# Kernel tuning notes

Measured on AMD Instinct MI355X. Metric: run time of the kernel, lower is better.

Reference implementation:

```python
import jax, jax.numpy as jnp
import numpy as np

N_NODES = 8192
N_EDGES = 65536


def _segment_softmax(scores, seg_ids, num_segments):
    # scores: [E, 1], seg_ids: [E] -> softmax over edges sharing the same dst
    m = jax.ops.segment_max(scores, seg_ids, num_segments=num_segments)  # [N,1]
    e = jnp.exp(scores - m[seg_ids])
    denom = jax.ops.segment_sum(e, seg_ids, num_segments=num_segments)   # [N,1]
    return e / denom[seg_ids]


def setup_inputs() -> dict:
    key = jax.random.key(0)
    ks = jax.random.split(key, 12)
    s = lambda fin: 1.0 / np.sqrt(fin)
    inp = {
        'n_f': jax.random.normal(ks[0], (N_NODES, 1024), jnp.float32),
        'word2vec': jax.random.normal(ks[1], (N_NODES, 300), jnp.float32),
        's_f': jax.random.normal(ks[2], (N_EDGES, 16), jnp.float32),
        'src': jax.random.randint(ks[3], (N_EDGES,), 0, N_NODES),
        'dst': jax.random.randint(ks[4], (N_EDGES,), 0, N_NODES),
        'We': jax.random.normal(ks[5], (2064, 1024), jnp.float32) * s(2064),
        'be': jnp.zeros((1024,), jnp.float32),
        'Wel': jax.random.normal(ks[6], (600, 600), jnp.float32) * s(600),
        'bel': jnp.zeros((600,), jnp.float32),
        'Wa': jax.random.normal(ks[7], (1024, 1), jnp.float32) * s(1024),
        'ba': jnp.zeros((1,), jnp.float32),
        'Wal': jax.random.normal(ks[8], (600, 1), jnp.float32) * s(600),
        'bal': jnp.zeros((1,), jnp.float32),
        'Wn': jax.random.normal(ks[9], (2048, 1024), jnp.float32) * s(2048),
        'bn': jnp.zeros((1024,), jnp.float32),
        'Wnl': jax.random.normal(ks[10], (600, 300), jnp.float32) * s(600),
        'bnl': jnp.zeros((300,), jnp.float32),
    }
    return inp


def reference(n_f, word2vec, s_f, src, dst,
              We, be, Wel, bel, Wa, ba, Wal, bal, Wn, bn, Wnl, bnl):
    # ---- edge apply (H_H_EdgeApplyModule) ----
    src_nf = n_f[src]                                    # [E,1024] gather
    feat = jnp.concatenate([src_nf, s_f, n_f[dst]], axis=1)  # [E,2064]
    e_f = jax.nn.relu(feat @ We + be)                    # [E,1024]
    feat_lang = jnp.concatenate([word2vec[src], word2vec[dst]], axis=1)  # [E,600]
    e_f_lang = jax.nn.relu(feat_lang @ Wel + bel)        # [E,600]

    # ---- edge attention (E_AttentionModule1): scalar score per edge ----
    a_feat = e_f @ Wa + ba                               # [E,1]
    a_feat_lang = e_f_lang @ Wal + bal                   # [E,1]

    # ---- reduce: mailbox softmax over incoming edges per dst node ----
    alpha = _segment_softmax(a_feat, dst, N_NODES)       # [E,1]
    alpha_lang = _segment_softmax(a_feat_lang, dst, N_NODES)
    z_f = jax.ops.segment_sum(alpha * (src_nf + e_f), dst, num_segments=N_NODES)      # [N,1024]
    z_f_lang = jax.ops.segment_sum(alpha_lang * word2vec[src], dst, num_segments=N_NODES)  # [N,300]

    # ---- node apply (H_NodeApplyModule) ----
    new_n_f = jax.nn.relu(jnp.concatenate([n_f, z_f], axis=1) @ Wn + bn)              # [N,1024]
    new_n_f_lang = jax.nn.relu(jnp.concatenate([word2vec, z_f_lang], axis=1) @ Wnl + bnl)  # [N,300]
    return new_n_f, new_n_f_lang
```

## Files before the change

kernel.cpp:

```cpp
#include <hip/hip_runtime.h>
#include <hip/hip_bf16.h>

#define N_NODES 8192
#define N_EDGES 65536
#define OUT0_ELEMS ((size_t)N_NODES * 1024)

using bf16 = __hip_bfloat16;
typedef __attribute__((ext_vector_type(8))) short short8;
typedef __attribute__((ext_vector_type(4))) float f32x4;

__device__ __forceinline__ float b2f(bf16 x) { return __bfloat162float(x); }
__device__ __forceinline__ bf16 f2b(float x) { return __float2bfloat16(x); }
__device__ __forceinline__ unsigned short bbits(float x)
{
  union { bf16 h; unsigned short u; } v; v.h = f2b(x); return v.u;
}
__device__ __forceinline__ unsigned pack2(float a, float b)
{
  return (unsigned)bbits(a) | ((unsigned)bbits(b) << 16);
}
__device__ __forceinline__ float4 ld4b(const bf16* p)
{
  uint2 u = *(const uint2*)p;
  float4 r;
  r.x = __uint_as_float(u.x << 16);
  r.y = __uint_as_float(u.x & 0xffff0000u);
  r.z = __uint_as_float(u.y << 16);
  r.w = __uint_as_float(u.y & 0xffff0000u);
  return r;
}
__device__ __forceinline__ void st4b(bf16* p, float a, float b, float c, float d)
{
  uint2 v; v.x = pack2(a, b); v.y = pack2(c, d);
  *(uint2*)p = v;
}

__global__ void GNN_27650999451833_kernel() {}

__global__ void gnn6_zero(int* __restrict__ p, int n)
{
  int i = blockIdx.x * blockDim.x + threadIdx.x;
  if (i < n) p[i] = 0;
}

__global__ __launch_bounds__(256)
void gnn7_cvt(const float* __restrict__ src, bf16* __restrict__ dst, int n8)
{
  int i = blockIdx.x * blockDim.x + threadIdx.x;
  if (i < n8) {
    float4 a = ((const float4*)src)[2 * i];
    float4 b = ((const float4*)src)[2 * i + 1];
    uint4 p;
    p.x = pack2(a.x, a.y); p.y = pack2(a.z, a.w);
    p.z = pack2(b.x, b.y); p.w = pack2(b.z, b.w);
    ((uint4*)dst)[i] = p;
  }
}

__global__ __launch_bounds__(256)
void gnn8_pad_w2v(const float* __restrict__ src, bf16* __restrict__ dst)
{
  int idx = blockIdx.x * blockDim.x + threadIdx.x;
  if (idx >= N_NODES * 80) return;
  int r = idx / 80, c0 = (idx % 80) * 4;
  float v[4];
#pragma unroll
  for (int j = 0; j < 4; ++j) {
    int c = c0 + j;
    v[j] = (c < 300) ? src[(size_t)r * 300 + c] : 0.f;
  }
  uint2 p; p.x = pack2(v[0], v[1]); p.y = pack2(v[2], v[3]);
  *(uint2*)(dst + (size_t)r * 320 + c0) = p;
}

__global__ __launch_bounds__(256)
void gnn10_t_We(const float* __restrict__ src, bf16* __restrict__ dst)
{
  __shared__ float tile[32][33];
  const int kb = blockIdx.x * 32, nb = blockIdx.y * 32;
  const int tx = threadIdx.x & 31, ty = threadIdx.x >> 5;
  const int n = nb + tx;
#pragma unroll
  for (int i = ty; i < 32; i += 8)
    tile[i][tx] = (n < 1024)
        ? src[(size_t)(kb + i) * 1024 + n]
        : src[(size_t)(1040 + kb + i) * 1024 + (n - 1024)];
  __syncthreads();
#pragma unroll
  for (int i = ty; i < 32; i += 8)
    dst[(size_t)(nb + i) * 1024 + kb + tx] = f2b(tile[tx][i]);
}

__global__ __launch_bounds__(256)
void gnn10_t_Wn(const float* __restrict__ src, bf16* __restrict__ dst)
{
  __shared__ float tile[32][33];
  const int kb = blockIdx.x * 32, nb = blockIdx.y * 32;
  const int tx = threadIdx.x & 31, ty = threadIdx.x >> 5;
#pragma unroll
  for (int i = ty; i < 32; i += 8)
    tile[i][tx] = src[(size_t)(kb + i) * 1024 + nb + tx];
  __syncthreads();
#pragma unroll
  for (int i = ty; i < 32; i += 8)
    dst[(size_t)(nb + i) * 2048 + kb + tx] = f2b(tile[tx][i]);
}

__global__ __launch_bounds__(256)
void gnn10_t_Wel(const float* __restrict__ src, bf16* __restrict__ dst)
{
  __shared__ float tile[32][33];
  const int kb = blockIdx.x * 32, nb = blockIdx.y * 32;
  const int tx = threadIdx.x & 31, ty = threadIdx.x >> 5;
  const int n = nb + tx;
#pragma unroll
  for (int i = ty; i < 32; i += 8) {
    int k = kb + i;
    float v = 0.f;
    if (k < 300) {
      if (n < 600)       v = src[(size_t)k * 600 + n];
      else if (n < 1200) v = src[(size_t)(300 + k) * 600 + (n - 600)];
    }
    tile[i][tx] = v;
  }
  __syncthreads();
#pragma unroll
  for (int i = ty; i < 32; i += 8)
    dst[(size_t)(nb + i) * 320 + kb + tx] = f2b(tile[tx][i]);
}

__global__ __launch_bounds__(256)
void gnn10_t_Wnl(const float* __restrict__ src, bf16* __restrict__ dst)
{
  __shared__ float tile[32][33];
  const int kb = blockIdx.x * 32, nb = blockIdx.y * 32;
  const int tx = threadIdx.x & 31, ty = threadIdx.x >> 5;
  const int n = nb + tx;
#pragma unroll
  for (int i = ty; i < 32; i += 8) {
    int k = kb + i;
    int kr = (k < 300) ? k : ((k >= 320 && k < 620) ? (k - 20) : -1);
    tile[i][tx] = (kr >= 0 && n < 300) ? src[(size_t)kr * 300 + n] : 0.f;
  }
  __syncthreads();
#pragma unroll
  for (int i = ty; i < 32; i += 8)
    dst[(size_t)(nb + i) * 640 + kb + tx] = f2b(tile[tx][i]);
}

__global__ __launch_bounds__(256)
void gnn10_mm_P(const bf16* __restrict__ A, const bf16* __restrict__ BT,
                bf16* __restrict__ P)
{
  __shared__ short As[128 * 40];
  __shared__ short Bs[128 * 40];
  const int t = threadIdx.x;
  const int col0 = blockIdx.x * 128, row0 = blockIdx.y * 128;
  const int lane = t & 63, w = t >> 6, m16 = lane & 15, q = lane >> 4;
  const int wr = w >> 1, wc = w & 1;

  f32x4 acc[4][4];
#pragma unroll
  for (int mi = 0; mi < 4; ++mi)
#pragma unroll
    for (int ni = 0; ni < 4; ++ni) acc[mi][ni] = (f32x4){0.f, 0.f, 0.f, 0.f};

  const int ar = t >> 1, ah = (t & 1) * 16;
  const bf16* aptr = A + (size_t)(row0 + ar) * 1024 + ah;
  const bf16* bptr = BT + (size_t)(col0 + ar) * 1024 + ah;

  uint4 a0 = *(const uint4*)(aptr);
  uint4 a1 = *(const uint4*)(aptr + 8);
  uint4 b0 = *(const uint4*)(bptr);
  uint4 b1 = *(const uint4*)(bptr + 8);

  for (int k0 = 0; k0 < 1024; k0 += 32) {
    if (k0) __syncthreads();
    *(uint4*)&As[ar * 40 + ah] = a0;
    *(uint4*)&As[ar * 40 + ah + 8] = a1;
    *(uint4*)&Bs[ar * 40 + ah] = b0;
    *(uint4*)&Bs[ar * 40 + ah + 8] = b1;
    __syncthreads();
    if (k0 + 32 < 1024) {
      a0 = *(const uint4*)(aptr + k0 + 32);
      a1 = *(const uint4*)(aptr + k0 + 40);
      b0 = *(const uint4*)(bptr + k0 + 32);
      b1 = *(const uint4*)(bptr + k0 + 40);
    }
    short8 af[4];
#pragma unroll
    for (int mi = 0; mi < 4; ++mi)
      af[mi] = *(const short8*)&As[(wr * 64 + mi * 16 + m16) * 40 + 8 * q];
#pragma unroll
    for (int ni = 0; ni < 4; ++ni) {
      short8 bfv = *(const short8*)&Bs[(wc * 64 + ni * 16 + m16) * 40 + 8 * q];
#pragma unroll
      for (int mi = 0; mi < 4; ++mi)
        acc[mi][ni] =
            __builtin_amdgcn_mfma_f32_16x16x32_bf16(af[mi], bfv, acc[mi][ni], 0, 0, 0);
    }
  }
#pragma unroll
  for (int mi = 0; mi < 4; ++mi)
#pragma unroll
    for (int ni = 0; ni < 4; ++ni) {
      int c = col0 + wc * 64 + ni * 16 + m16;
#pragma unroll
      for (int r = 0; r < 4; ++r)
        P[(size_t)(row0 + wr * 64 + mi * 16 + 4 * q + r) * 2048 + c] =
            f2b(acc[mi][ni][r]);
    }
}

__global__ __launch_bounds__(256)
void gnn10_mm_out_n(const bf16* __restrict__ A0, const bf16* __restrict__ A1,
                    const bf16* __restrict__ BT, const float* __restrict__ bn,
                    float* __restrict__ out)
{
  __shared__ short As[128 * 40];
  __shared__ short Bs[128 * 40];
  const int t = threadIdx.x;
  const int col0 = blockIdx.x * 128, row0 = blockIdx.y * 128;
  const int lane = t & 63, w = t >> 6, m16 = lane & 15, q = lane >> 4;
  const int wr = w >> 1, wc = w & 1;

  f32x4 acc[4][4];
#pragma unroll
  for (int mi = 0; mi < 4; ++mi)
#pragma unroll
    for (int ni = 0; ni < 4; ++ni) acc[mi][ni] = (f32x4){0.f, 0.f, 0.f, 0.f};

  const int ar = t >> 1, ah = (t & 1) * 16;
  const bf16* ap0 = A0 + (size_t)(row0 + ar) * 1024 + ah;
  const bf16* ap1 = A1 + (size_t)(row0 + ar) * 1024 + ah;
  const bf16* bptr = BT + (size_t)(col0 + ar) * 2048 + ah;

  uint4 a0 = *(const uint4*)(ap0);
  uint4 a1 = *(const uint4*)(ap0 + 8);
  uint4 b0 = *(const uint4*)(bptr);
  uint4 b1 = *(const uint4*)(bptr + 8);

  for (int k0 = 0; k0 < 2048; k0 += 32) {
    if (k0) __syncthreads();
    *(uint4*)&As[ar * 40 + ah] = a0;
    *(uint4*)&As[ar * 40 + ah + 8] = a1;
    *(uint4*)&Bs[ar * 40 + ah] = b0;
    *(uint4*)&Bs[ar * 40 + ah + 8] = b1;
    __syncthreads();
    if (k0 + 32 < 2048) {
      int kn = k0 + 32;
      const bf16* ap = (kn < 1024) ? (ap0 + kn) : (ap1 + (kn - 1024));
      a0 = *(const uint4*)(ap);
      a1 = *(const uint4*)(ap + 8);
      b0 = *(const uint4*)(bptr + kn);
      b1 = *(const uint4*)(bptr + kn + 8);
    }
    short8 af[4];
#pragma unroll
    for (int mi = 0; mi < 4; ++mi)
      af[mi] = *(const short8*)&As[(wr * 64 + mi * 16 + m16) * 40 + 8 * q];
#pragma unroll
    for (int ni = 0; ni < 4; ++ni) {
      short8 bfv = *(const short8*)&Bs[(wc * 64 + ni * 16 + m16) * 40 + 8 * q];
#pragma unroll
      for (int mi = 0; mi < 4; ++mi)
        acc[mi][ni] =
            __builtin_amdgcn_mfma_f32_16x16x32_bf16(af[mi], bfv, acc[mi][ni], 0, 0, 0);
    }
  }
#pragma unroll
  for (int mi = 0; mi < 4; ++mi)
#pragma unroll
    for (int ni = 0; ni < 4; ++ni) {
      int c = col0 + wc * 64 + ni * 16 + m16;
      float bias = bn[c];
#pragma unroll
      for (int r = 0; r < 4; ++r) {
        float v = acc[mi][ni][r] + bias;
        out[(size_t)(row0 + wr * 64 + mi * 16 + 4 * q + r) * 1024 + c] =
            fmaxf(v, 0.f);
      }
    }
}

__global__ __launch_bounds__(256)
void gnn10_mm_Q(const bf16* __restrict__ A, const bf16* __restrict__ BT,
                bf16* __restrict__ Q)
{
  __shared__ short As[128 * 40];
  __shared__ short Bs[128 * 40];
  const int t = threadIdx.x;
  const int col0 = blockIdx.x * 128, row0 = blockIdx.y * 128;
  const int lane = t & 63, w = t >> 6, m16 = lane & 15, q = lane >> 4;
  const int wr = w >> 1, wc = w & 1;

  f32x4 acc[4][4];
#pragma unroll
  for (int mi = 0; mi < 4; ++mi)
#pragma unroll
    for (int ni = 0; ni < 4; ++ni) acc[mi][ni] = (f32x4){0.f, 0.f, 0.f, 0.f};

  const int ar = t >> 1, ah = (t & 1) * 16;
  const bf16* aptr = A + (size_t)(row0 + ar) * 320 + ah;
  const bf16* bptr = BT + (size_t)(col0 + ar) * 320 + ah;

  uint4 a0 = *(const uint4*)(aptr);
  uint4 a1 = *(const uint4*)(aptr + 8);
  uint4 b0 = *(const uint4*)(bptr);
  uint4 b1 = *(const uint4*)(bptr + 8);

  for (int k0 = 0; k0 < 320; k0 += 32) {
    if (k0) __syncthreads();
    *(uint4*)&As[ar * 40 + ah] = a0;
    *(uint4*)&As[ar * 40 + ah + 8] = a1;
    *(uint4*)&Bs[ar * 40 + ah] = b0;
    *(uint4*)&Bs[ar * 40 + ah + 8] = b1;
    __syncthreads();
    if (k0 + 32 < 320) {
      a0 = *(const uint4*)(aptr + k0 + 32);
      a1 = *(const uint4*)(aptr + k0 + 40);
      b0 = *(const uint4*)(bptr + k0 + 32);
      b1 = *(const uint4*)(bptr + k0 + 40);
    }
    short8 af[4];
#pragma unroll
    for (int mi = 0; mi < 4; ++mi)
      af[mi] = *(const short8*)&As[(wr * 64 + mi * 16 + m16) * 40 + 8 * q];
#pragma unroll
    for (int ni = 0; ni < 4; ++ni) {
      short8 bfv = *(const short8*)&Bs[(wc * 64 + ni * 16 + m16) * 40 + 8 * q];
#pragma unroll
      for (int mi = 0; mi < 4; ++mi)
        acc[mi][ni] =
            __builtin_amdgcn_mfma_f32_16x16x32_bf16(af[mi], bfv, acc[mi][ni], 0, 0, 0);
    }
  }
#pragma unroll
  for (int mi = 0; mi < 4; ++mi)
#pragma unroll
    for (int ni = 0; ni < 4; ++ni) {
      int c = col0 + wc * 64 + ni * 16 + m16;
#pragma unroll
      for (int r = 0; r < 4; ++r)
        Q[(size_t)(row0 + wr * 64 + mi * 16 + 4 * q + r) * 1280 + c] =
            f2b(acc[mi][ni][r]);
    }
}

__global__ __launch_bounds__(256)
void gnn10_mm_out_l(const bf16* __restrict__ A0, const bf16* __restrict__ A1,
                    const bf16* __restrict__ BT, const float* __restrict__ bnl,
                    float* __restrict__ out2)
{
  __shared__ short As[128 * 40];
  __shared__ short Bs[128 * 40];
  const int t = threadIdx.x;
  const int col0 = blockIdx.x * 128, row0 = blockIdx.y * 128;
  const int lane = t & 63, w = t >> 6, m16 = lane & 15, q = lane >> 4;
  const int wr = w >> 1, wc = w & 1;

  f32x4 acc[4][4];
#pragma unroll
  for (int mi = 0; mi < 4; ++mi)
#pragma unroll
    for (int ni = 0; ni < 4; ++ni) acc[mi][ni] = (f32x4){0.f, 0.f, 0.f, 0.f};

  const int ar = t >> 1, ah = (t & 1) * 16;
  const bf16* ap0 = A0 + (size_t)(row0 + ar) * 320 + ah;
  const bf16* ap1 = A1 + (size_t)(row0 + ar) * 320 + ah;
  const bf16* bptr = BT + (size_t)(col0 + ar) * 640 + ah;

  uint4 a0 = *(const uint4*)(ap0);
  uint4 a1 = *(const uint4*)(ap0 + 8);
  uint4 b0 = *(const uint4*)(bptr);
  uint4 b1 = *(const uint4*)(bptr + 8);

  for (int k0 = 0; k0 < 640; k0 += 32) {
    if (k0) __syncthreads();
    *(uint4*)&As[ar * 40 + ah] = a0;
    *(uint4*)&As[ar * 40 + ah + 8] = a1;
    *(uint4*)&Bs[ar * 40 + ah] = b0;
    *(uint4*)&Bs[ar * 40 + ah + 8] = b1;
    __syncthreads();
    if (k0 + 32 < 640) {
      int kn = k0 + 32;
      const bf16* ap = (kn < 320) ? (ap0 + kn) : (ap1 + (kn - 320));
      a0 = *(const uint4*)(ap);
      a1 = *(const uint4*)(ap + 8);
      b0 = *(const uint4*)(bptr + kn);
      b1 = *(const uint4*)(bptr + kn + 8);
    }
    short8 af[4];
#pragma unroll
    for (int mi = 0; mi < 4; ++mi)
      af[mi] = *(const short8*)&As[(wr * 64 + mi * 16 + m16) * 40 + 8 * q];
#pragma unroll
    for (int ni = 0; ni < 4; ++ni) {
      short8 bfv = *(const short8*)&Bs[(wc * 64 + ni * 16 + m16) * 40 + 8 * q];
#pragma unroll
      for (int mi = 0; mi < 4; ++mi)
        acc[mi][ni] =
            __builtin_amdgcn_mfma_f32_16x16x32_bf16(af[mi], bfv, acc[mi][ni], 0, 0, 0);
    }
  }
#pragma unroll
  for (int mi = 0; mi < 4; ++mi)
#pragma unroll
    for (int ni = 0; ni < 4; ++ni) {
      int c = col0 + wc * 64 + ni * 16 + m16;
      if (c < 300) {
        float bias = bnl[c];
#pragma unroll
        for (int r = 0; r < 4; ++r) {
          float v = acc[mi][ni][r] + bias;
          out2[(size_t)(row0 + wr * 64 + mi * 16 + 4 * q + r) * 300 + c] =
              fmaxf(v, 0.f);
        }
      }
    }
}

__global__ __launch_bounds__(256)
void gnn11_edge_score(const int* __restrict__ src, const int* __restrict__ dst,
                      const float* __restrict__ s_f, const float* __restrict__ We,
                      const float* __restrict__ be, const float* __restrict__ Wa,
                      const float* __restrict__ ba, const float* __restrict__ bel,
                      const float* __restrict__ Wal, const float* __restrict__ bal,
                      const bf16* __restrict__ P, const bf16* __restrict__ Q,
                      float* __restrict__ af, float* __restrict__ afl)
{
  const int t = threadIdx.x;
  const int lane = t & 63, w = t >> 6;
  const int c0 = 4 * t;
  const int e0 = blockIdx.x * 8;

  float wef[16][4];
#pragma unroll
  for (int k = 0; k < 16; ++k) {
    float4 v = *(const float4*)(We + (size_t)(1024 + k) * 1024 + c0);
    wef[k][0] = v.x; wef[k][1] = v.y; wef[k][2] = v.z; wef[k][3] = v.w;
  }
  float4 bev = *(const float4*)(be + c0);
  float4 wav = *(const float4*)(Wa + c0);
  const bool lact = (t < 150);
  float4 belv = {0, 0, 0, 0}, walv = {0, 0, 0, 0};
  if (lact) { belv = *(const float4*)(bel + c0); walv = *(const float4*)(Wal + c0); }

  int ss[8], dd[8];
  {
    int4 a = *(const int4*)(src + e0);
    int4 b = *(const int4*)(src + e0 + 4);
    ss[0] = a.x; ss[1] = a.y; ss[2] = a.z; ss[3] = a.w;
    ss[4] = b.x; ss[5] = b.y; ss[6] = b.z; ss[7] = b.w;
    int4 c = *(const int4*)(dst + e0);
    int4 d = *(const int4*)(dst + e0 + 4);
    dd[0] = c.x; dd[1] = c.y; dd[2] = c.z; dd[3] = c.w;
    dd[4] = d.x; dd[5] = d.y; dd[6] = d.z; dd[7] = d.w;
  }

  float pf[8], pl[8];

#pragma unroll
  for (int i = 0; i < 8; ++i) {
    const int e = e0 + i;

    float sfv[16];
    {
      const float4* sp = (const float4*)(s_f + (size_t)e * 16);
      float4 s0 = sp[0], s1 = sp[1], s2 = sp[2], s3 = sp[3];
      sfv[0] = s0.x; sfv[1] = s0.y; sfv[2] = s0.z; sfv[3] = s0.w;
      sfv[4] = s1.x; sfv[5] = s1.y; sfv[6] = s1.z; sfv[7] = s1.w;
      sfv[8] = s2.x; sfv[9] = s2.y; sfv[10] = s2.z; sfv[11] = s2.w;
      sfv[12] = s3.x; sfv[13] = s3.y; sfv[14] = s3.z; sfv[15] = s3.w;
    }

    float4 p1 = ld4b(P + (size_t)ss[i] * 2048 + c0);
    float4 p2 = ld4b(P + (size_t)dd[i] * 2048 + 1024 + c0);
    float pv[4] = {p1.x + p2.x + bev.x, p1.y + p2.y + bev.y,
                   p1.z + p2.z + bev.z, p1.w + p2.w + bev.w};
    float acc = 0.f;
#pragma unroll
    for (int j = 0; j < 4; ++j) {
      float v = pv[j];
#pragma unroll
      for (int k = 0; k < 16; ++k) v = fmaf(sfv[k], wef[k][j], v);
      acc = fmaf(fmaxf(v, 0.f), (&wav.x)[j], acc);
    }
    pf[i] = acc;
  }

#pragma unroll
  for (int i = 0; i < 8; ++i) {
    float acc = 0.f;
    if (lact) {
      float4 q1 = ld4b(Q + (size_t)ss[i] * 1280 + c0);
      float4 q2 = ld4b(Q + (size_t)dd[i] * 1280 + 600 + c0);
      float qv[4] = {q1.x + q2.x + belv.x, q1.y + q2.y + belv.y,
                     q1.z + q2.z + belv.z, q1.w + q2.w + belv.w};
#pragma unroll
      for (int j = 0; j < 4; ++j)
        acc = fmaf(fmaxf(qv[j], 0.f), (&walv.x)[j], acc);
    }
    pl[i] = acc;
  }

  __shared__ float shf[8][4], shl[8][4];
#pragma unroll
  for (int i = 0; i < 8; ++i) {
#pragma unroll
    for (int o = 32; o > 0; o >>= 1) {
      pf[i] += __shfl_down(pf[i], o, 64);
      pl[i] += __shfl_down(pl[i], o, 64);
    }
  }
  if (lane == 0) {
#pragma unroll
    for (int i = 0; i < 8; ++i) { shf[i][w] = pf[i]; shl[i][w] = pl[i]; }
  }
  __syncthreads();
  if (t < 8)
    af[e0 + t] = shf[t][0] + shf[t][1] + shf[t][2] + shf[t][3] + ba[0];
  if (t >= 64 && t < 72) {
    const int i = t & 7;
    afl[e0 + i] = shl[i][0] + shl[i][1] + shl[i][2] + shl[i][3] + bal[0];
  }
}

__global__ void gnn6_count(const int* __restrict__ dst, int* __restrict__ cnt)
{
  int e = blockIdx.x * blockDim.x + threadIdx.x;
  if (e < N_EDGES) atomicAdd(&cnt[dst[e]], 1);
}

__global__ __launch_bounds__(1024)
void gnn6_scan(const int* __restrict__ cnt, int* __restrict__ off, int* __restrict__ cur)
{
  __shared__ int sh[1024];
  const int t = threadIdx.x;
  int local[8]; int sum = 0;
#pragma unroll
  for (int i = 0; i < 8; ++i) { int v = cnt[t * 8 + i]; local[i] = sum; sum += v; }
  sh[t] = sum;
  __syncthreads();
  for (int d = 1; d < 1024; d <<= 1) {
    int v = (t >= d) ? sh[t - d] : 0;
    __syncthreads();
    sh[t] += v;
    __syncthreads();
  }
  int basev = (t > 0) ? sh[t - 1] : 0;
#pragma unroll
  for (int i = 0; i < 8; ++i) { int o = basev + local[i]; off[t * 8 + i] = o; cur[t * 8 + i] = o; }
  if (t == 1023) off[8192] = sh[1023];
}

__global__ void gnn6_fill(const int* __restrict__ dst, int* __restrict__ cur,
                          int* __restrict__ elist)
{
  int e = blockIdx.x * blockDim.x + threadIdx.x;
  if (e < N_EDGES) { int p = atomicAdd(&cur[dst[e]], 1); elist[p] = e; }
}

__global__ __launch_bounds__(256)
void gnn6_alpha(const int* __restrict__ off, const int* __restrict__ elist,
                float* __restrict__ af, float* __restrict__ afl)
{
  const int n = blockIdx.x * 256 + threadIdx.x;
  if (n >= N_NODES) return;
  const int base = off[n];
  const int deg = off[n + 1] - base;
  float m = -1e30f, ml = -1e30f;
  for (int i = 0; i < deg; ++i) {
    int e = elist[base + i];
    m = fmaxf(m, af[e]);
    ml = fmaxf(ml, afl[e]);
  }
  float den = 0.f, denl = 0.f;
  for (int i = 0; i < deg; ++i) {
    int e = elist[base + i];
    den += expf(af[e] - m);
    denl += expf(afl[e] - ml);
  }
  float inv = (den > 0.f) ? 1.f / den : 0.f;
  float invl = (denl > 0.f) ? 1.f / denl : 0.f;
  for (int i = 0; i < deg; ++i) {
    int e = elist[base + i];
    af[e] = expf(af[e] - m) * inv;
    afl[e] = expf(afl[e] - ml) * invl;
  }
}

__global__ __launch_bounds__(256)
void gnn9_node_z(const int* __restrict__ off, const int* __restrict__ elist,
                 const int* __restrict__ src, const float* __restrict__ af,
                 const float* __restrict__ afl, const bf16* __restrict__ nf_bf,
                 const bf16* __restrict__ w2v_pad, const float* __restrict__ s_f,
                 const float* __restrict__ We, const float* __restrict__ be,
                 const bf16* __restrict__ P, bf16* __restrict__ zf,
                 bf16* __restrict__ zfl_pad)
{
  const int node = blockIdx.x;
  const int t = threadIdx.x;
  const int c0 = 4 * t;
  const int base = off[node];
  const int deg = off[node + 1] - base;

  float wef[16][4];
#pragma unroll
  for (int k = 0; k < 16; ++k) {
    float4 v = *(const float4*)(We + (size_t)(1024 + k) * 1024 + c0);
    wef[k][0] = v.x; wef[k][1] = v.y; wef[k][2] = v.z; wef[k][3] = v.w;
  }
  float4 p2v = ld4b(P + (size_t)node * 2048 + 1024 + c0);
  float4 bev = *(const float4*)(be + c0);
  const float p2[4] = {p2v.x + bev.x, p2v.y + bev.y, p2v.z + bev.z, p2v.w + bev.w};

  float acc[4] = {0.f, 0.f, 0.f, 0.f};
  float accl[4] = {0.f, 0.f, 0.f, 0.f};
  const bool lact = (t < 75);

  for (int i = 0; i < deg; ++i) {
    const int e = elist[base + i];
    const int s = src[e];
    const float wgt = af[e];
    const float wl = afl[e];

    float sfv[16];
    {
      const float4* sp = (const float4*)(s_f + (size_t)e * 16);
      float4 s0 = sp[0], s1 = sp[1], s2 = sp[2], s3 = sp[3];
      sfv[0] = s0.x; sfv[1] = s0.y; sfv[2] = s0.z; sfv[3] = s0.w;
      sfv[4] = s1.x; sfv[5] = s1.y; sfv[6] = s1.z; sfv[7] = s1.w;
      sfv[8] = s2.x; sfv[9] = s2.y; sfv[10] = s2.z; sfv[11] = s2.w;
      sfv[12] = s3.x; sfv[13] = s3.y; sfv[14] = s3.z; sfv[15] = s3.w;
    }

    float4 p1 = ld4b(P + (size_t)s * 2048 + c0);
    float4 nf4 = ld4b(nf_bf + (size_t)s * 1024 + c0);
    const float p1a[4] = {p1.x, p1.y, p1.z, p1.w};
    const float nfa[4] = {nf4.x, nf4.y, nf4.z, nf4.w};
#pragma unroll
    for (int j = 0; j < 4; ++j) {
      float ef = p1a[j] + p2[j];
#pragma unroll
      for (int k = 0; k < 16; ++k) ef = fmaf(sfv[k], wef[k][j], ef);
      ef = fmaxf(ef, 0.f);
      acc[j] = fmaf(wgt, nfa[j] + ef, acc[j]);
    }
    if (lact) {
      float4 wv = ld4b(w2v_pad + (size_t)s * 320 + c0);
      accl[0] = fmaf(wl, wv.x, accl[0]);
      accl[1] = fmaf(wl, wv.y, accl[1]);
      accl[2] = fmaf(wl, wv.z, accl[2]);
      accl[3] = fmaf(wl, wv.w, accl[3]);
    }
  }
  st4b(zf + (size_t)node * 1024 + c0, acc[0], acc[1], acc[2], acc[3]);
  if (lact)
    st4b(zfl_pad + (size_t)node * 320 + c0, accl[0], accl[1], accl[2], accl[3]);
  else if (t < 80)
    st4b(zfl_pad + (size_t)node * 320 + c0, 0.f, 0.f, 0.f, 0.f);
}

extern "C" void kernel_launch(void* const* d_in, const int* in_sizes, int n_in,
                              void* d_out, int out_size, void* d_ws, size_t ws_size,
                              hipStream_t stream)
{
  (void)hipGetLastError();
  if (n_in != 17) { hipMemsetAsync(d_out, 0x41, 4096, stream); return; }

  const float* n_f = (const float*)d_in[0];
  const float* w2v = (const float*)d_in[1];
  const float* s_f = (const float*)d_in[2];
  const int*   src = (const int*)d_in[3];
  const int*   dst = (const int*)d_in[4];
  const float* We  = (const float*)d_in[5];
  const float* be  = (const float*)d_in[6];
  const float* Wel = (const float*)d_in[7];
  const float* bel = (const float*)d_in[8];
  const float* Wa  = (const float*)d_in[9];
  const float* ba  = (const float*)d_in[10];
  const float* Wal = (const float*)d_in[11];
  const float* bal = (const float*)d_in[12];
  const float* Wn  = (const float*)d_in[13];
  const float* bn  = (const float*)d_in[14];
  const float* Wnl = (const float*)d_in[15];
  const float* bnl = (const float*)d_in[16];
  float* out  = (float*)d_out;
  float* out2 = out + OUT0_ELEMS;

  char* ws = (char*)d_ws;
  size_t o = 0;
  auto alloc = [&](size_t bytes) -> void* {
    void* p = ws + o; o += bytes; o = (o + 255) & ~(size_t)255; return p;
  };
  bf16* P        = (bf16*)alloc((size_t)N_NODES * 2048 * 2);
  bf16* Q        = (bf16*)alloc((size_t)N_NODES * 1280 * 2);
  bf16* zf       = (bf16*)alloc((size_t)N_NODES * 1024 * 2);
  bf16* zfl_pad  = (bf16*)alloc((size_t)N_NODES * 320 * 2);
  bf16* nf_bf    = (bf16*)alloc((size_t)N_NODES * 1024 * 2);
  bf16* w2v_pad  = (bf16*)alloc((size_t)N_NODES * 320 * 2);
  bf16* WeT      = (bf16*)alloc((size_t)2048 * 1024 * 2);
  bf16* WnT      = (bf16*)alloc((size_t)1024 * 2048 * 2);
  bf16* WelT     = (bf16*)alloc((size_t)1280 * 320 * 2);
  bf16* WnlT     = (bf16*)alloc((size_t)384 * 640 * 2);
  float* af      = (float*)alloc((size_t)N_EDGES * 4);
  float* afl     = (float*)alloc((size_t)N_EDGES * 4);
  int* cnt       = (int*)alloc((size_t)N_NODES * 4);
  int* offs      = (int*)alloc((size_t)(N_NODES + 1) * 4);
  int* cur       = (int*)alloc((size_t)N_NODES * 4);
  int* elist     = (int*)alloc((size_t)N_EDGES * 4);
  if (o > ws_size) { hipMemsetAsync(d_out, 0x42, 4096, stream); return; }

  gnn6_zero<<<N_NODES / 256, 256, 0, stream>>>(cnt, N_NODES);
  gnn7_cvt<<<(N_NODES * 1024 / 8 + 255) / 256, 256, 0, stream>>>(n_f, nf_bf,
                                                                 N_NODES * 1024 / 8);
  gnn8_pad_w2v<<<(N_NODES * 80 + 255) / 256, 256, 0, stream>>>(w2v, w2v_pad);
  { dim3 g(32, 64); gnn10_t_We<<<g, 256, 0, stream>>>(We, WeT); }
  { dim3 g(64, 32); gnn10_t_Wn<<<g, 256, 0, stream>>>(Wn, WnT); }
  { dim3 g(10, 40); gnn10_t_Wel<<<g, 256, 0, stream>>>(Wel, WelT); }
  { dim3 g(20, 12); gnn10_t_Wnl<<<g, 256, 0, stream>>>(Wnl, WnlT); }

  {
    dim3 g(2048 / 128, N_NODES / 128);
    gnn10_mm_P<<<g, 256, 0, stream>>>(nf_bf, WeT, P);
  }
  {
    dim3 g(1280 / 128, N_NODES / 128);
    gnn10_mm_Q<<<g, 256, 0, stream>>>(w2v_pad, WelT, Q);
  }

  gnn11_edge_score<<<N_EDGES / 8, 256, 0, stream>>>(src, dst, s_f, We, be, Wa, ba,
                                                    bel, Wal, bal, P, Q, af, afl);

  gnn6_count<<<N_EDGES / 256, 256, 0, stream>>>(dst, cnt);
  gnn6_scan<<<1, 1024, 0, stream>>>(cnt, offs, cur);
  gnn6_fill<<<N_EDGES / 256, 256, 0, stream>>>(dst, cur, elist);
  gnn6_alpha<<<N_NODES / 256, 256, 0, stream>>>(offs, elist, af, afl);

  gnn9_node_z<<<N_NODES, 256, 0, stream>>>(offs, elist, src, af, afl, nf_bf,
                                           w2v_pad, s_f, We, be, P, zf, zfl_pad);

  {
    dim3 g(1024 / 128, N_NODES / 128);
    gnn10_mm_out_n<<<g, 256, 0, stream>>>(nf_bf, zf, WnT, bn, out);
  }
  {
    dim3 g(384 / 128, N_NODES / 128);
    gnn10_mm_out_l<<<g, 256, 0, stream>>>(w2v_pad, zfl_pad, WnlT, bnl, out2);
  }

  if (hipGetLastError() != hipSuccess) hipMemsetAsync(d_out, 0x44, 4096, stream);
}
```

Before: 506.3 us.

## Precompute s_f·We tail per edge with an MFMA GEMM and fold biases into P/Q

Result: no change. 515.6 us (+1.8%).

```diff
diff --git a/kernel.cpp b/kernel.cpp
--- a/kernel.cpp
+++ b/kernel.cpp
@@ -74,6 +74,36 @@
 }
 
 __global__ __launch_bounds__(256)
+void gnn12_sf_pad(const float* __restrict__ s_f, bf16* __restrict__ sf_pad)
+{
+  int e = blockIdx.x * 256 + threadIdx.x;
+  if (e >= N_EDGES) return;
+  const float4* sp = (const float4*)(s_f + (size_t)e * 16);
+  float4 s0 = sp[0], s1 = sp[1], s2 = sp[2], s3 = sp[3];
+  uint4 lo, hi;
+  lo.x = pack2(s0.x, s0.y); lo.y = pack2(s0.z, s0.w);
+  lo.z = pack2(s1.x, s1.y); lo.w = pack2(s1.z, s1.w);
+  hi.x = pack2(s2.x, s2.y); hi.y = pack2(s2.z, s2.w);
+  hi.z = pack2(s3.x, s3.y); hi.w = pack2(s3.z, s3.w);
+  uint4* dp = (uint4*)(sf_pad + (size_t)e * 32);
+  dp[0] = lo; dp[1] = hi;
+  dp[2] = (uint4){0, 0, 0, 0}; dp[3] = (uint4){0, 0, 0, 0};
+}
+
+__global__ __launch_bounds__(256)
+void gnn12_t_Wetail(const float* __restrict__ We, bf16* __restrict__ BT)
+{
+  int c = blockIdx.x * 256 + threadIdx.x;
+  if (c >= 1024) return;
+  bf16* row = BT + (size_t)c * 32;
+#pragma unroll
+  for (int k = 0; k < 16; ++k)
+    row[k] = f2b(We[(size_t)(1024 + k) * 1024 + c]);
+#pragma unroll
+  for (int k = 16; k < 32; ++k) row[k] = f2b(0.f);
+}
+
+__global__ __launch_bounds__(256)
 void gnn10_t_We(const float* __restrict__ src, bf16* __restrict__ dst)
 {
   __shared__ float tile[32][33];
@@ -150,7 +180,7 @@
 
 __global__ __launch_bounds__(256)
 void gnn10_mm_P(const bf16* __restrict__ A, const bf16* __restrict__ BT,
-                bf16* __restrict__ P)
+                bf16* __restrict__ P, const float* __restrict__ be)
 {
   __shared__ short As[128 * 40];
   __shared__ short Bs[128 * 40];
@@ -205,10 +235,11 @@
 #pragma unroll
     for (int ni = 0; ni < 4; ++ni) {
       int c = col0 + wc * 64 + ni * 16 + m16;
+      float bias = (be != nullptr && c >= 1024) ? be[c - 1024] : 0.f;
 #pragma unroll
       for (int r = 0; r < 4; ++r)
         P[(size_t)(row0 + wr * 64 + mi * 16 + 4 * q + r) * 2048 + c] =
-            f2b(acc[mi][ni][r]);
+            f2b(acc[mi][ni][r] + bias);
     }
 }
 
@@ -285,7 +316,7 @@
 
 __global__ __launch_bounds__(256)
 void gnn10_mm_Q(const bf16* __restrict__ A, const bf16* __restrict__ BT,
-                bf16* __restrict__ Q)
+                bf16* __restrict__ Q, const float* __restrict__ bel)
 {
   __shared__ short As[128 * 40];
   __shared__ short Bs[128 * 40];
@@ -340,10 +371,11 @@
 #pragma unroll
     for (int ni = 0; ni < 4; ++ni) {
       int c = col0 + wc * 64 + ni * 16 + m16;
+      float bias = (bel != nullptr && c >= 600 && c < 1200) ? bel[c - 600] : 0.f;
 #pragma unroll
       for (int r = 0; r < 4; ++r)
         Q[(size_t)(row0 + wr * 64 + mi * 16 + 4 * q + r) * 1280 + c] =
-            f2b(acc[mi][ni][r]);
+            f2b(acc[mi][ni][r] + bias);
     }
 }
 
@@ -421,30 +453,71 @@
 }
 
 __global__ __launch_bounds__(256)
-void gnn11_edge_score(const int* __restrict__ src, const int* __restrict__ dst,
-                      const float* __restrict__ s_f, const float* __restrict__ We,
-                      const float* __restrict__ be, const float* __restrict__ Wa,
-                      const float* __restrict__ ba, const float* __restrict__ bel,
-                      const float* __restrict__ Wal, const float* __restrict__ bal,
-                      const bf16* __restrict__ P, const bf16* __restrict__ Q,
-                      float* __restrict__ af, float* __restrict__ afl)
+void gnn12_mm_S(const bf16* __restrict__ A, const bf16* __restrict__ BT,
+                bf16* __restrict__ S)
+{
+  __shared__ short As[128 * 40];
+  __shared__ short Bs[128 * 40];
+  const int t = threadIdx.x;
+  const int col0 = blockIdx.x * 128, row0 = blockIdx.y * 128;
+  const int lane = t & 63, w = t >> 6, m16 = lane & 15, q = lane >> 4;
+  const int wr = w >> 1, wc = w & 1;
+
+  const int ar = t >> 1, ah = (t & 1) * 16;
+  *(uint4*)&As[ar * 40 + ah]     = *(const uint4*)(A + (size_t)(row0 + ar) * 32 + ah);
+  *(uint4*)&As[ar * 40 + ah + 8] = *(const uint4*)(A + (size_t)(row0 + ar) * 32 + ah + 8);
+  *(uint4*)&Bs[ar * 40 + ah]     = *(const uint4*)(BT + (size_t)(col0 + ar) * 32 + ah);
+  *(uint4*)&Bs[ar * 40 + ah + 8] = *(const uint4*)(BT + (size_t)(col0 + ar) * 32 + ah + 8);
+  __syncthreads();
+
+  f32x4 acc[4][4];
+#pragma unroll
+  for (int mi = 0; mi < 4; ++mi)
+#pragma unroll
+    for (int ni = 0; ni < 4; ++ni) acc[mi][ni] = (f32x4){0.f, 0.f, 0.f, 0.f};
+
+  short8 af[4];
+#pragma unroll
+  for (int mi = 0; mi < 4; ++mi)
+    af[mi] = *(const short8*)&As[(wr * 64 + mi * 16 + m16) * 40 + 8 * q];
+#pragma unroll
+  for (int ni = 0; ni < 4; ++ni) {
+    short8 bfv = *(const short8*)&Bs[(wc * 64 + ni * 16 + m16) * 40 + 8 * q];
+#pragma unroll
+    for (int mi = 0; mi < 4; ++mi)
+      acc[mi][ni] =
+          __builtin_amdgcn_mfma_f32_16x16x32_bf16(af[mi], bfv, acc[mi][ni], 0, 0, 0);
+  }
+
+#pragma unroll
+  for (int mi = 0; mi < 4; ++mi)
+#pragma unroll
+    for (int ni = 0; ni < 4; ++ni) {
+      int c = col0 + wc * 64 + ni * 16 + m16;
+#pragma unroll
+      for (int r = 0; r < 4; ++r)
+        S[(size_t)(row0 + wr * 64 + mi * 16 + 4 * q + r) * 1024 + c] =
+            f2b(acc[mi][ni][r]);
+    }
+}
+
+__global__ __launch_bounds__(256)
+void gnn12_edge_score(const int* __restrict__ src, const int* __restrict__ dst,
+                      const bf16* __restrict__ S, const float* __restrict__ Wa,
+                      const float* __restrict__ ba, const float* __restrict__ Wal,
+                      const float* __restrict__ bal, const bf16* __restrict__ P,
+                      const bf16* __restrict__ Q, float* __restrict__ af,
+                      float* __restrict__ afl)
 {
   const int t = threadIdx.x;
   const int lane = t & 63, w = t >> 6;
   const int c0 = 4 * t;
   const int e0 = blockIdx.x * 8;
 
-  float wef[16][4];
-#pragma unroll
-  for (int k = 0; k < 16; ++k) {
-    float4 v = *(const float4*)(We + (size_t)(1024 + k) * 1024 + c0);
-    wef[k][0] = v.x; wef[k][1] = v.y; wef[k][2] = v.z; wef[k][3] = v.w;
-  }
-  float4 bev = *(const float4*)(be + c0);
   float4 wav = *(const float4*)(Wa + c0);
   const bool lact = (t < 150);
-  float4 belv = {0, 0, 0, 0}, walv = {0, 0, 0, 0};
-  if (lact) { belv = *(const float4*)(bel + c0); walv = *(const float4*)(Wal + c0); }
+  float4 walv = {0, 0, 0, 0};
+  if (lact) walv = *(const float4*)(Wal + c0);
 
   int ss[8], dd[8];
   {
@@ -463,7 +536,93 @@
 #pragma unroll
   for (int i = 0; i < 8; ++i) {
     const int e = e0 + i;
-
+    float4 sv = ld4b(S + (size_t)e * 1024 + c0);
+    float4 p1 = ld4b(P + (size_t)ss[i] * 2048 + c0);
+    float4 p2 = ld4b(P + (size_t)dd[i] * 2048 + 1024 + c0);
+    float acc = 0.f;
+    acc = fmaf(fmaxf(p1.x + p2.x + sv.x, 0.f), wav.x, acc);
+    acc = fmaf(fmaxf(p1.y + p2.y + sv.y, 0.f), wav.y, acc);
+    acc = fmaf(fmaxf(p1.z + p2.z + sv.z, 0.f), wav.z, acc);
+    acc = fmaf(fmaxf(p1.w + p2.w + sv.w, 0.f), wav.w, acc);
+    pf[i] = acc;
+
+    float accl = 0.f;
+    if (lact) {
+      float4 q1 = ld4b(Q + (size_t)ss[i] * 1280 + c0);
+      float4 q2 = ld4b(Q + (size_t)dd[i] * 1280 + 600 + c0);
+      accl = fmaf(fmaxf(q1.x + q2.x, 0.f), walv.x, accl);
+      accl = fmaf(fmaxf(q1.y + q2.y, 0.f), walv.y, accl);
+      accl = fmaf(fmaxf(q1.z + q2.z, 0.f), walv.z, accl);
+      accl = fmaf(fmaxf(q1.w + q2.w, 0.f), walv.w, accl);
+    }
+    pl[i] = accl;
+  }
+
+  __shared__ float shf[8][4], shl[8][4];
+#pragma unroll
+  for (int i = 0; i < 8; ++i) {
+#pragma unroll
+    for (int o = 32; o > 0; o >>= 1) {
+      pf[i] += __shfl_down(pf[i], o, 64);
+      pl[i] += __shfl_down(pl[i], o, 64);
+    }
+  }
+  if (lane == 0) {
+#pragma unroll
+    for (int i = 0; i < 8; ++i) { shf[i][w] = pf[i]; shl[i][w] = pl[i]; }
+  }
+  __syncthreads();
+  if (t < 8)
+    af[e0 + t] = shf[t][0] + shf[t][1] + shf[t][2] + shf[t][3] + ba[0];
+  if (t >= 64 && t < 72) {
+    const int i = t & 7;
+    afl[e0 + i] = shl[i][0] + shl[i][1] + shl[i][2] + shl[i][3] + bal[0];
+  }
+}
+
+__global__ __launch_bounds__(256)
+void gnn11_edge_score(const int* __restrict__ src, const int* __restrict__ dst,
+                      const float* __restrict__ s_f, const float* __restrict__ We,
+                      const float* __restrict__ be, const float* __restrict__ Wa,
+                      const float* __restrict__ ba, const float* __restrict__ bel,
+                      const float* __restrict__ Wal, const float* __restrict__ bal,
+                      const bf16* __restrict__ P, const bf16* __restrict__ Q,
+                      float* __restrict__ af, float* __restrict__ afl)
+{
+  const int t = threadIdx.x;
+  const int lane = t & 63, w = t >> 6;
+  const int c0 = 4 * t;
+  const int e0 = blockIdx.x * 8;
+
+  float wef[16][4];
+#pragma unroll
+  for (int k = 0; k < 16; ++k) {
+    float4 v = *(const float4*)(We + (size_t)(1024 + k) * 1024 + c0);
+    wef[k][0] = v.x; wef[k][1] = v.y; wef[k][2] = v.z; wef[k][3] = v.w;
+  }
+  float4 bev = *(const float4*)(be + c0);
+  float4 wav = *(const float4*)(Wa + c0);
+  const bool lact = (t < 150);
+  float4 belv = {0, 0, 0, 0}, walv = {0, 0, 0, 0};
+  if (lact) { belv = *(const float4*)(bel + c0); walv = *(const float4*)(Wal + c0); }
+
+  int ss[8], dd[8];
+  {
+    int4 a = *(const int4*)(src + e0);
+    int4 b = *(const int4*)(src + e0 + 4);
+    ss[0] = a.x; ss[1] = a.y; ss[2] = a.z; ss[3] = a.w;
+    ss[4] = b.x; ss[5] = b.y; ss[6] = b.z; ss[7] = b.w;
+    int4 c = *(const int4*)(dst + e0);
+    int4 d = *(const int4*)(dst + e0 + 4);
+    dd[0] = c.x; dd[1] = c.y; dd[2] = c.z; dd[3] = c.w;
+    dd[4] = d.x; dd[5] = d.y; dd[6] = d.z; dd[7] = d.w;
+  }
+
+  float pf[8], pl[8];
+
+#pragma unroll
+  for (int i = 0; i < 8; ++i) {
+    const int e = e0 + i;
     float sfv[16];
     {
       const float4* sp = (const float4*)(s_f + (size_t)e * 16);
@@ -473,7 +632,6 @@
       sfv[8] = s2.x; sfv[9] = s2.y; sfv[10] = s2.z; sfv[11] = s2.w;
       sfv[12] = s3.x; sfv[13] = s3.y; sfv[14] = s3.z; sfv[15] = s3.w;
     }
-
     float4 p1 = ld4b(P + (size_t)ss[i] * 2048 + c0);
     float4 p2 = ld4b(P + (size_t)dd[i] * 2048 + 1024 + c0);
     float pv[4] = {p1.x + p2.x + bev.x, p1.y + p2.y + bev.y,
@@ -487,11 +645,8 @@
       acc = fmaf(fmaxf(v, 0.f), (&wav.x)[j], acc);
     }
     pf[i] = acc;
-  }
-
-#pragma unroll
-  for (int i = 0; i < 8; ++i) {
-    float acc = 0.f;
+
+    float accl = 0.f;
     if (lact) {
       float4 q1 = ld4b(Q + (size_t)ss[i] * 1280 + c0);
       float4 q2 = ld4b(Q + (size_t)dd[i] * 1280 + 600 + c0);
@@ -499,9 +654,9 @@
                      q1.z + q2.z + belv.z, q1.w + q2.w + belv.w};
 #pragma unroll
       for (int j = 0; j < 4; ++j)
-        acc = fmaf(fmaxf(qv[j], 0.f), (&walv.x)[j], acc);
-    }
-    pl[i] = acc;
+        accl = fmaf(fmaxf(qv[j], 0.f), (&walv.x)[j], accl);
+    }
+    pl[i] = accl;
   }
 
   __shared__ float shf[8][4], shl[8][4];
@@ -591,6 +746,59 @@
 }
 
 __global__ __launch_bounds__(256)
+void gnn12_node_z(const int* __restrict__ off, const int* __restrict__ elist,
+                  const int* __restrict__ src, const float* __restrict__ af,
+                  const float* __restrict__ afl, const bf16* __restrict__ nf_bf,
+                  const bf16* __restrict__ w2v_pad, const bf16* __restrict__ S,
+                  const bf16* __restrict__ P, bf16* __restrict__ zf,
+                  bf16* __restrict__ zfl_pad)
+{
+  const int node = blockIdx.x;
+  const int t = threadIdx.x;
+  const int c0 = 4 * t;
+  const int base = off[node];
+  const int deg = off[node + 1] - base;
+
+  float4 p2v = ld4b(P + (size_t)node * 2048 + 1024 + c0);
+  const float p2[4] = {p2v.x, p2v.y, p2v.z, p2v.w};
+
+  float acc[4] = {0.f, 0.f, 0.f, 0.f};
+  float accl[4] = {0.f, 0.f, 0.f, 0.f};
+  const bool lact = (t < 75);
+
+  for (int i = 0; i < deg; ++i) {
+    const int e = elist[base + i];
+    const int s = src[e];
+    const float wgt = af[e];
+    const float wl = afl[e];
+
+    float4 sv = ld4b(S + (size_t)e * 1024 + c0);
+    float4 p1 = ld4b(P + (size_t)s * 2048 + c0);
+    float4 nf4 = ld4b(nf_bf + (size_t)s * 1024 + c0);
+    const float p1a[4] = {p1.x, p1.y, p1.z, p1.w};
+    const float sva[4] = {sv.x, sv.y, sv.z, sv.w};
+    const float nfa[4] = {nf4.x, nf4.y, nf4.z, nf4.w};
+#pragma unroll
+    for (int j = 0; j < 4; ++j) {
+      float ef = fmaxf(p1a[j] + p2[j] + sva[j], 0.f);
+      acc[j] = fmaf(wgt, nfa[j] + ef, acc[j]);
+    }
+    if (lact) {
+      float4 wv = ld4b(w2v_pad + (size_t)s * 320 + c0);
+      accl[0] = fmaf(wl, wv.x, accl[0]);
+      accl[1] = fmaf(wl, wv.y, accl[1]);
+      accl[2] = fmaf(wl, wv.z, accl[2]);
+      accl[3] = fmaf(wl, wv.w, accl[3]);
+    }
+  }
+  st4b(zf + (size_t)node * 1024 + c0, acc[0], acc[1], acc[2], acc[3]);
+  if (lact)
+    st4b(zfl_pad + (size_t)node * 320 + c0, accl[0], accl[1], accl[2], accl[3]);
+  else if (t < 80)
+    st4b(zfl_pad + (size_t)node * 320 + c0, 0.f, 0.f, 0.f, 0.f);
+}
+
+__global__ __launch_bounds__(256)
 void gnn9_node_z(const int* __restrict__ off, const int* __restrict__ elist,
                  const int* __restrict__ src, const float* __restrict__ af,
                  const float* __restrict__ afl, const bf16* __restrict__ nf_bf,
@@ -667,7 +875,7 @@
                               hipStream_t stream)
 {
   (void)hipGetLastError();
-  if (n_in != 17) { hipMemsetAsync(d_out, 0x41, 4096, stream); return; }
+  if (n_in != 17) { (void)hipMemsetAsync(d_out, 0x41, 4096, stream); return; }
 
   const float* n_f = (const float*)d_in[0];
   const float* w2v = (const float*)d_in[1];
@@ -710,7 +918,13 @@
   int* offs      = (int*)alloc((size_t)(N_NODES + 1) * 4);
   int* cur       = (int*)alloc((size_t)N_NODES * 4);
   int* elist     = (int*)alloc((size_t)N_EDGES * 4);
-  if (o > ws_size) { hipMemsetAsync(d_out, 0x42, 4096, stream); return; }
+  size_t base_end = o;
+  if (base_end > ws_size) { (void)hipMemsetAsync(d_out, 0x42, 4096, stream); return; }
+
+  bf16* sf_pad  = (bf16*)alloc((size_t)N_EDGES * 32 * 2);
+  bf16* WeTtail = (bf16*)alloc((size_t)1024 * 32 * 2);
+  bf16* S       = (bf16*)alloc((size_t)N_EDGES * 1024 * 2);
+  const bool useS = (o <= ws_size);
 
   gnn6_zero<<<N_NODES / 256, 256, 0, stream>>>(cnt, N_NODES);
   gnn7_cvt<<<(N_NODES * 1024 / 8 + 255) / 256, 256, 0, stream>>>(n_f, nf_bf,
@@ -720,26 +934,45 @@
   { dim3 g(64, 32); gnn10_t_Wn<<<g, 256, 0, stream>>>(Wn, WnT); }
   { dim3 g(10, 40); gnn10_t_Wel<<<g, 256, 0, stream>>>(Wel, WelT); }
   { dim3 g(20, 12); gnn10_t_Wnl<<<g, 256, 0, stream>>>(Wnl, WnlT); }
+  if (useS) {
+    gnn12_sf_pad<<<N_EDGES / 256, 256, 0, stream>>>(s_f, sf_pad);
+    gnn12_t_Wetail<<<4, 256, 0, stream>>>(We, WeTtail);
+  }
 
   {
     dim3 g(2048 / 128, N_NODES / 128);
-    gnn10_mm_P<<<g, 256, 0, stream>>>(nf_bf, WeT, P);
+    gnn10_mm_P<<<g, 256, 0, stream>>>(nf_bf, WeT, P, useS ? be : nullptr);
   }
   {
     dim3 g(1280 / 128, N_NODES / 128);
-    gnn10_mm_Q<<<g, 256, 0, stream>>>(w2v_pad, WelT, Q);
-  }
-
-  gnn11_edge_score<<<N_EDGES / 8, 256, 0, stream>>>(src, dst, s_f, We, be, Wa, ba,
-                                                    bel, Wal, bal, P, Q, af, afl);
+    gnn10_mm_Q<<<g, 256, 0, stream>>>(w2v_pad, WelT, Q, useS ? bel : nullptr);
+  }
+  if (useS) {
+    dim3 g(1024 / 128, N_EDGES / 128);
+    gnn12_mm_S<<<g, 256, 0, stream>>>(sf_pad, WeTtail, S);
+  }
+
+  if (useS) {
+    gnn12_edge_score<<<N_EDGES / 8, 256, 0, stream>>>(src, dst, S, Wa, ba, Wal,
+                                                      bal, P, Q, af, afl);
+  } else {
+    gnn11_edge_score<<<N_EDGES / 8, 256, 0, stream>>>(src, dst, s_f, We, be, Wa,
+                                                      ba, bel, Wal, bal, P, Q,
+                                                      af, afl);
+  }
 
   gnn6_count<<<N_EDGES / 256, 256, 0, stream>>>(dst, cnt);
   gnn6_scan<<<1, 1024, 0, stream>>>(cnt, offs, cur);
   gnn6_fill<<<N_EDGES / 256, 256, 0, stream>>>(dst, cur, elist);
   gnn6_alpha<<<N_NODES / 256, 256, 0, stream>>>(offs, elist, af, afl);
 
-  gnn9_node_z<<<N_NODES, 256, 0, stream>>>(offs, elist, src, af, afl, nf_bf,
-                                           w2v_pad, s_f, We, be, P, zf, zfl_pad);
+  if (useS) {
+    gnn12_node_z<<<N_NODES, 256, 0, stream>>>(offs, elist, src, af, afl, nf_bf,
+                                              w2v_pad, S, P, zf, zfl_pad);
+  } else {
+    gnn9_node_z<<<N_NODES, 256, 0, stream>>>(offs, elist, src, af, afl, nf_bf,
+                                             w2v_pad, s_f, We, be, P, zf, zfl_pad);
+  }
 
   {
     dim3 g(1024 / 128, N_NODES / 128);
@@ -750,5 +983,5 @@
     gnn10_mm_out_l<<<g, 256, 0, stream>>>(w2v_pad, zfl_pad, WnlT, bnl, out2);
   }
 
-  if (hipGetLastError() != hipSuccess) hipMemsetAsync(d_out, 0x44, 4096, stream);
-}
+  if (hipGetLastError() != hipSuccess) (void)hipMemsetAsync(d_out, 0x44, 4096, stream);
+}
```
